# Kernel optimization log

Measured on AMD Instinct MI355X. Metric: run time of the kernel, lower is better.

The kernel has to match this reference:

```python
import jax, jax.numpy as jnp
import numpy as np

T = 8  # number of DP iterations (self.T)

def setup_inputs() -> dict:
    key = jax.random.key(0)
    ks = jax.random.split(key, 9)
    bs, dims, L, d = 16, 4, 2048, 256
    x = jax.random.uniform(ks[0], (bs, dims, L), dtype=jnp.float32)  # one-hot-like input
    s_in = 1.0 / np.sqrt(dims)
    s_d = 1.0 / np.sqrt(d)
    W1 = jax.random.uniform(ks[1], (d, dims), minval=-s_in, maxval=s_in, dtype=jnp.float32)
    b1 = jax.random.uniform(ks[2], (d,), minval=-s_in, maxval=s_in, dtype=jnp.float32)
    W2 = jax.random.uniform(ks[3], (d, d), minval=-s_d, maxval=s_d, dtype=jnp.float32)
    b2 = jax.random.uniform(ks[4], (d,), minval=-s_d, maxval=s_d, dtype=jnp.float32)
    W3 = jax.random.uniform(ks[5], (d, dims), minval=-s_in, maxval=s_in, dtype=jnp.float32)
    b3 = jax.random.uniform(ks[6], (d,), minval=-s_in, maxval=s_in, dtype=jnp.float32)
    W4 = jax.random.uniform(ks[7], (d, d), minval=-s_d, maxval=s_d, dtype=jnp.float32)
    b4 = jax.random.uniform(ks[8], (d,), minval=-s_d, maxval=s_d, dtype=jnp.float32)
    return dict(x=x, W1=W1, b1=b1, W2=W2, b2=b2, W3=W3, b3=b3, W4=W4, b4=b4)

def reference(x, W1, b1, W2, b2, W3, b3, W4, b4):
    # x: (bs, dims, L). The original allocates V:(bs,T+1,L+2,L+2,d) but only the
    # two diagonals V[i,j,j+1] ("up") and V[i,j,j-1] ("down") are ever written/read,
    # so the recurrence collapses to two (bs,L,d) lanes.
    a = jnp.einsum('bdl,od->blo', x, W1) + b1  # W1(x_j) for all j: (bs, L, d)
    bs, L, d = a.shape
    zcol = jnp.zeros((bs, 1, d), a.dtype)
    shift_r = lambda v: jnp.concatenate([zcol, v[:, :-1]], axis=1)  # v[j-1], zero at j=0
    shift_l = lambda v: jnp.concatenate([v[:, 1:], zcol], axis=1)   # v[j+1], zero at j=L-1
    up = jnp.zeros_like(a)   # up[j]   = V[i, j+1, j+2] (0-indexed lane)
    down = jnp.zeros_like(a) # down[j] = V[i, j+1, j]
    for _ in range(T):
        up = jax.nn.relu(a + shift_r(up) @ W2.T + b2)
        down = jax.nn.relu(a + shift_l(down) @ W2.T + b2)
    c = jnp.einsum('bdl,od->blo', x, W3) + b3
    # miu[j] = relu(W3 x_j + W4(V[T,j-1,j]) + W4(V[T,j+1,j]))
    miu = jax.nn.relu(c + (shift_r(up) @ W4.T + b4) + (shift_l(down) @ W4.T + b4))
    return miu  # (bs, L, d)
```

## Files before the change

kernel.cpp:

```cpp
#include <hip/hip_runtime.h>


typedef __bf16 bf16x8 __attribute__((ext_vector_type(8)));
typedef __bf16 bf16x4 __attribute__((ext_vector_type(4)));
typedef float f32x16 __attribute__((ext_vector_type(16)));

#define MFMA32(a, b, c) __builtin_amdgcn_mfma_f32_32x32x16_bf16(a, b, c, 0, 0, 0)

__device__ __forceinline__ unsigned short f2bf(float f) {
  unsigned int u = __builtin_bit_cast(unsigned int, f);
  u += 0x7fffu + ((u >> 16) & 1u);
  return (unsigned short)(u >> 16);
}

#define STATE_OFF 139264

__global__ void prep_kernel(const float* __restrict__ W1, const float* __restrict__ b1,
                            const float* __restrict__ W2, const float* __restrict__ b2,
                            const float* __restrict__ W3, const float* __restrict__ b3,
                            const float* __restrict__ W4, const float* __restrict__ b4,
                            unsigned short* __restrict__ ws) {
  int idx = blockIdx.x * 256 + threadIdx.x;
  if (idx >= 139264) return;
  float v = 0.0f;
  if (idx < 131072) {
    const float* W = (idx < 65536) ? W2 : W4;
    int i = idx & 65535;
    int j = i & 7, f = i >> 3;
    int lane = f & 63, slot = f >> 6;
    int ks = slot & 15, ot = slot >> 4;
    int o = ot * 32 + (lane & 31);
    int k = ks * 16 + (lane >> 5) * 8 + j;
    v = W[o * 256 + k];
  } else {
    int i = idx - 131072;
    bool first = (i < 4096);
    int ii = i & 4095;
    int j = ii & 7, f = ii >> 3;
    int lane = f & 63, ot = f >> 6;
    int o = ot * 32 + (lane & 31);
    if (lane < 32) {
      if (j < 4) v = first ? W1[o * 4 + j] : W3[o * 4 + j];
      else if (j == 4) v = first ? (b1[o] + b2[o]) : (b3[o] + 2.0f * b4[o]);
    }
  }
  ws[idx] = f2bf(v);
}

__global__ __launch_bounds__(256, 2)
void chain_kernel(const float* __restrict__ x, unsigned short* __restrict__ ws) {
  __shared__ int4 U[64 * 32];
  __shared__ int4 xw[80];
  __shared__ int4 zc;

  const int tid = threadIdx.x;
  const int l = tid & 63;
  const int w = tid >> 6;
  const int lane31 = l & 31;
  const int khalf = l >> 5;
  const int phase = blockIdx.x >> 9;
  const int tile = blockIdx.x & 511;
  const int b = tile >> 5;
  const int j0 = (tile & 31) * 64;

  const int4* w2f = (const int4*)ws;
  const int4* w1xg = (const int4*)(ws + 131072);

  if (tid == 0) zc = make_int4(0, 0, 0, 0);
  if (tid < 80) {
    int j = j0 - 8 + tid;
    int4 c = make_int4(0, 0, 0, 0);
    if (j >= 0 && j < 2048) {
      const float* xb = x + (b * 4) * 2048 + j;
      unsigned short h0 = f2bf(xb[0]);
      unsigned short h1 = f2bf(xb[2048]);
      unsigned short h2 = f2bf(xb[4096]);
      unsigned short h3 = f2bf(xb[6144]);
      c = make_int4((int)(h0 | ((unsigned int)h1 << 16)),
                    (int)(h2 | ((unsigned int)h3 << 16)),
                    0x00003f80, 0);
    }
    xw[tid] = c;
  }

  const int ot0 = w * 2;
  bf16x8 w2c[2][8];
  bf16x8 w1x[2];
#pragma unroll
  for (int t2 = 0; t2 < 2; ++t2) {
    w1x[t2] = __builtin_bit_cast(bf16x8, w1xg[(ot0 + t2) * 64 + l]);
#pragma unroll
    for (int ks = 0; ks < 8; ++ks)
      w2c[t2][ks] = __builtin_bit_cast(bf16x8, w2f[((ot0 + t2) * 16 + ks) * 64 + l]);
  }
  __syncthreads();

  const int mrow0 = lane31;
  const int mrow1 = 32 + lane31;

#pragma unroll 1
  for (int t = 1; t <= 8; ++t) {
    f32x16 acc[2][2] = {};
#pragma unroll
    for (int mt = 0; mt < 2; ++mt) {
      int m = mt ? mrow1 : mrow0;
      int widx = (phase == 0) ? (m + t - 1) : (m + 17 - t);
      const int4* p = (l < 32) ? (xw + widx) : (&zc);
      bf16x8 bx = __builtin_bit_cast(bf16x8, *p);
      acc[mt][0] = MFMA32(w1x[0], bx, acc[mt][0]);
      acc[mt][1] = MFMA32(w1x[1], bx, acc[mt][1]);
    }
    if (t > 1) {
#pragma unroll
      for (int ks = 0; ks < 16; ++ks) {
        int c0 = 2 * ks + khalf;
        bf16x8 bu0 = __builtin_bit_cast(bf16x8, U[mrow0 * 32 + (c0 ^ (mrow0 & 7))]);
        bf16x8 bu1 = __builtin_bit_cast(bf16x8, U[mrow1 * 32 + (c0 ^ (mrow1 & 7))]);
        bf16x8 af0, af1;
        if (ks < 8) { af0 = w2c[0][ks]; af1 = w2c[1][ks]; }
        else {
          af0 = __builtin_bit_cast(bf16x8, w2f[(ot0 * 16 + ks) * 64 + l]);
          af1 = __builtin_bit_cast(bf16x8, w2f[((ot0 + 1) * 16 + ks) * 64 + l]);
        }
        acc[0][0] = MFMA32(af0, bu0, acc[0][0]);
        acc[0][1] = MFMA32(af1, bu0, acc[0][1]);
        acc[1][0] = MFMA32(af0, bu1, acc[1][0]);
        acc[1][1] = MFMA32(af1, bu1, acc[1][1]);
      }
    }
    __syncthreads();
#pragma unroll
    for (int mt = 0; mt < 2; ++mt) {
      int row = mt ? mrow1 : mrow0;
#pragma unroll
      for (int t2 = 0; t2 < 2; ++t2) {
        int ot = ot0 + t2;
#pragma unroll
        for (int q = 0; q < 4; ++q) {
          bf16x4 h;
          h.x = (__bf16)fmaxf(acc[mt][t2][4 * q + 0], 0.0f);
          h.y = (__bf16)fmaxf(acc[mt][t2][4 * q + 1], 0.0f);
          h.z = (__bf16)fmaxf(acc[mt][t2][4 * q + 2], 0.0f);
          h.w = (__bf16)fmaxf(acc[mt][t2][4 * q + 3], 0.0f);
          int co = ot * 4 + q;
          int coff = row * 32 + (co ^ (row & 7));
          *(uint2*)((char*)(U + coff) + khalf * 8) = __builtin_bit_cast(uint2, h);
        }
      }
    }
    __syncthreads();
  }

  int4* stg = (int4*)(ws + STATE_OFF) + (phase * 512 + tile) * 2048;
#pragma unroll
  for (int i = 0; i < 8; ++i) stg[i * 256 + tid] = U[i * 256 + tid];
}

__global__ __launch_bounds__(256, 2)
void final_kernel(const float* __restrict__ x, const unsigned short* __restrict__ ws,
                  float* __restrict__ out) {
  __shared__ int4 S[2][64 * 32];
  __shared__ int4 xw[64];
  __shared__ int4 zc;

  const int tid = threadIdx.x;
  const int l = tid & 63;
  const int w = tid >> 6;
  const int lane31 = l & 31;
  const int khalf = l >> 5;
  const int tile = blockIdx.x;
  const int b = tile >> 5;
  const int j0 = (tile & 31) * 64;

  const int4* w4f = (const int4*)(ws + 65536);
  const int4* w3xg = (const int4*)(ws + 135168);
  const int4* stg = (const int4*)(ws + STATE_OFF);

  if (tid == 0) zc = make_int4(0, 0, 0, 0);
  if (tid < 64) {
    int j = j0 + tid;
    const float* xb = x + (b * 4) * 2048 + j;
    unsigned short h0 = f2bf(xb[0]);
    unsigned short h1 = f2bf(xb[2048]);
    unsigned short h2 = f2bf(xb[4096]);
    unsigned short h3 = f2bf(xb[6144]);
    xw[tid] = make_int4((int)(h0 | ((unsigned int)h1 << 16)),
                        (int)(h2 | ((unsigned int)h3 << 16)),
                        0x00003f80, 0);
  }
#pragma unroll
  for (int i = 0; i < 8; ++i) {
    S[0][i * 256 + tid] = stg[tile * 2048 + i * 256 + tid];
    S[1][i * 256 + tid] = stg[(512 + tile) * 2048 + i * 256 + tid];
  }
  __syncthreads();

  const int ot0 = w * 2;
  const int mrow0 = lane31;
  const int mrow1 = 32 + lane31;

  f32x16 acc[2][2] = {};
  bf16x8 w3x0 = __builtin_bit_cast(bf16x8, w3xg[ot0 * 64 + l]);
  bf16x8 w3x1 = __builtin_bit_cast(bf16x8, w3xg[(ot0 + 1) * 64 + l]);
#pragma unroll
  for (int mt = 0; mt < 2; ++mt) {
    int m = mt ? mrow1 : mrow0;
    const int4* p = (l < 32) ? (xw + m) : (&zc);
    bf16x8 bx = __builtin_bit_cast(bf16x8, *p);
    acc[mt][0] = MFMA32(w3x0, bx, acc[mt][0]);
    acc[mt][1] = MFMA32(w3x1, bx, acc[mt][1]);
  }
#pragma unroll 1
  for (int ph = 0; ph < 2; ++ph) {
    const int4* Sp = S[ph];
#pragma unroll
    for (int ks = 0; ks < 16; ++ks) {
      int c0 = 2 * ks + khalf;
      bf16x8 bu0 = __builtin_bit_cast(bf16x8, Sp[mrow0 * 32 + (c0 ^ (mrow0 & 7))]);
      bf16x8 bu1 = __builtin_bit_cast(bf16x8, Sp[mrow1 * 32 + (c0 ^ (mrow1 & 7))]);
      bf16x8 af0 = __builtin_bit_cast(bf16x8, w4f[(ot0 * 16 + ks) * 64 + l]);
      bf16x8 af1 = __builtin_bit_cast(bf16x8, w4f[((ot0 + 1) * 16 + ks) * 64 + l]);
      acc[0][0] = MFMA32(af0, bu0, acc[0][0]);
      acc[0][1] = MFMA32(af1, bu0, acc[0][1]);
      acc[1][0] = MFMA32(af0, bu1, acc[1][0]);
      acc[1][1] = MFMA32(af1, bu1, acc[1][1]);
    }
  }
#pragma unroll
  for (int mt = 0; mt < 2; ++mt) {
    int m = mt ? mrow1 : mrow0;
    int pbase = (b * 2048 + j0 + m) * 256;
#pragma unroll
    for (int t2 = 0; t2 < 2; ++t2) {
#pragma unroll
      for (int q = 0; q < 4; ++q) {
        int ob = (ot0 + t2) * 32 + 8 * q + 4 * khalf;
        float4 v;
        v.x = fmaxf(acc[mt][t2][4 * q + 0], 0.0f);
        v.y = fmaxf(acc[mt][t2][4 * q + 1], 0.0f);
        v.z = fmaxf(acc[mt][t2][4 * q + 2], 0.0f);
        v.w = fmaxf(acc[mt][t2][4 * q + 3], 0.0f);
        *(float4*)(out + pbase + ob) = v;
      }
    }
  }
}

extern "C" void kernel_launch(void* const* d_in, const int* in_sizes, int n_in,
                              void* d_out, int out_size, void* d_ws, size_t ws_size,
                              hipStream_t stream) {
  const float* x  = (const float*)d_in[0];
  const float* W1 = (const float*)d_in[1];
  const float* b1 = (const float*)d_in[2];
  const float* W2 = (const float*)d_in[3];
  const float* b2 = (const float*)d_in[4];
  const float* W3 = (const float*)d_in[5];
  const float* b3 = (const float*)d_in[6];
  const float* W4 = (const float*)d_in[7];
  const float* b4 = (const float*)d_in[8];
  unsigned short* ws = (unsigned short*)d_ws;

  prep_kernel<<<544, 256, 0, stream>>>(W1, b1, W2, b2, W3, b3, W4, b4, ws);
  chain_kernel<<<1024, 256, 0, stream>>>(x, ws);
  final_kernel<<<512, 256, 0, stream>>>(x, ws, (float*)d_out);
}
```

Measured before the change: 154.4 us.

## Re-partition chain kernel waves to keep full W2 slice in registers

Changes the per-wave work split in the chain kernel. Before, each wave covered 2 output tiles across both 32-row halves and reloaded half of its W2 fragments from global memory every iteration. Now each wave covers 4 output tiles for a single 32-row half, so its whole W2 slice (64 bf16x8 fragments) stays in registers and the per-step global reloads go away. In exchange, register pressure rises a lot under launch_bounds(256,2) and could spill. Each wave also reads half as many U rows from LDS.

```diff
diff --git a/kernel.cpp b/kernel.cpp
--- a/kernel.cpp
+++ b/kernel.cpp
@@ -58,6 +58,8 @@
   const int w = tid >> 6;
   const int lane31 = l & 31;
   const int khalf = l >> 5;
+  const int otg = w >> 1;
+  const int mhalf = w & 1;
   const int phase = blockIdx.x >> 9;
   const int tile = blockIdx.x & 511;
   const int b = tile >> 5;
@@ -83,69 +85,55 @@
     xw[tid] = c;
   }
 
-  const int ot0 = w * 2;
-  bf16x8 w2c[2][8];
-  bf16x8 w1x[2];
-#pragma unroll
-  for (int t2 = 0; t2 < 2; ++t2) {
-    w1x[t2] = __builtin_bit_cast(bf16x8, w1xg[(ot0 + t2) * 64 + l]);
-#pragma unroll
-    for (int ks = 0; ks < 8; ++ks)
-      w2c[t2][ks] = __builtin_bit_cast(bf16x8, w2f[((ot0 + t2) * 16 + ks) * 64 + l]);
+  bf16x8 w2c[4][16];
+  bf16x8 w1x[4];
+#pragma unroll
+  for (int i = 0; i < 4; ++i) {
+    int ot = otg * 4 + i;
+    w1x[i] = __builtin_bit_cast(bf16x8, w1xg[ot * 64 + l]);
+#pragma unroll
+    for (int ks = 0; ks < 16; ++ks)
+      w2c[i][ks] = __builtin_bit_cast(bf16x8, w2f[(ot * 16 + ks) * 64 + l]);
   }
   __syncthreads();
 
-  const int mrow0 = lane31;
-  const int mrow1 = 32 + lane31;
+  const int mrow = mhalf * 32 + lane31;
 
 #pragma unroll 1
   for (int t = 1; t <= 8; ++t) {
-    f32x16 acc[2][2] = {};
-#pragma unroll
-    for (int mt = 0; mt < 2; ++mt) {
-      int m = mt ? mrow1 : mrow0;
-      int widx = (phase == 0) ? (m + t - 1) : (m + 17 - t);
+    f32x16 acc[4] = {};
+    {
+      int widx = (phase == 0) ? (mrow + t - 1) : (mrow + 17 - t);
       const int4* p = (l < 32) ? (xw + widx) : (&zc);
       bf16x8 bx = __builtin_bit_cast(bf16x8, *p);
-      acc[mt][0] = MFMA32(w1x[0], bx, acc[mt][0]);
-      acc[mt][1] = MFMA32(w1x[1], bx, acc[mt][1]);
+#pragma unroll
+      for (int i = 0; i < 4; ++i) acc[i] = MFMA32(w1x[i], bx, acc[i]);
     }
     if (t > 1) {
 #pragma unroll
       for (int ks = 0; ks < 16; ++ks) {
         int c0 = 2 * ks + khalf;
-        bf16x8 bu0 = __builtin_bit_cast(bf16x8, U[mrow0 * 32 + (c0 ^ (mrow0 & 7))]);
-        bf16x8 bu1 = __builtin_bit_cast(bf16x8, U[mrow1 * 32 + (c0 ^ (mrow1 & 7))]);
-        bf16x8 af0, af1;
-        if (ks < 8) { af0 = w2c[0][ks]; af1 = w2c[1][ks]; }
-        else {
-          af0 = __builtin_bit_cast(bf16x8, w2f[(ot0 * 16 + ks) * 64 + l]);
-          af1 = __builtin_bit_cast(bf16x8, w2f[((ot0 + 1) * 16 + ks) * 64 + l]);
-        }
-        acc[0][0] = MFMA32(af0, bu0, acc[0][0]);
-        acc[0][1] = MFMA32(af1, bu0, acc[0][1]);
-        acc[1][0] = MFMA32(af0, bu1, acc[1][0]);
-        acc[1][1] = MFMA32(af1, bu1, acc[1][1]);
+        bf16x8 bu = __builtin_bit_cast(bf16x8, U[mrow * 32 + (c0 ^ (mrow & 7))]);
+        acc[0] = MFMA32(w2c[0][ks], bu, acc[0]);
+        acc[1] = MFMA32(w2c[1][ks], bu, acc[1]);
+        acc[2] = MFMA32(w2c[2][ks], bu, acc[2]);
+        acc[3] = MFMA32(w2c[3][ks], bu, acc[3]);
       }
     }
     __syncthreads();
 #pragma unroll
-    for (int mt = 0; mt < 2; ++mt) {
-      int row = mt ? mrow1 : mrow0;
-#pragma unroll
-      for (int t2 = 0; t2 < 2; ++t2) {
-        int ot = ot0 + t2;
-#pragma unroll
-        for (int q = 0; q < 4; ++q) {
-          bf16x4 h;
-          h.x = (__bf16)fmaxf(acc[mt][t2][4 * q + 0], 0.0f);
-          h.y = (__bf16)fmaxf(acc[mt][t2][4 * q + 1], 0.0f);
-          h.z = (__bf16)fmaxf(acc[mt][t2][4 * q + 2], 0.0f);
-          h.w = (__bf16)fmaxf(acc[mt][t2][4 * q + 3], 0.0f);
-          int co = ot * 4 + q;
-          int coff = row * 32 + (co ^ (row & 7));
-          *(uint2*)((char*)(U + coff) + khalf * 8) = __builtin_bit_cast(uint2, h);
-        }
+    for (int i = 0; i < 4; ++i) {
+      int ot = otg * 4 + i;
+#pragma unroll
+      for (int q = 0; q < 4; ++q) {
+        bf16x4 h;
+        h.x = (__bf16)fmaxf(acc[i][4 * q + 0], 0.0f);
+        h.y = (__bf16)fmaxf(acc[i][4 * q + 1], 0.0f);
+        h.z = (__bf16)fmaxf(acc[i][4 * q + 2], 0.0f);
+        h.w = (__bf16)fmaxf(acc[i][4 * q + 3], 0.0f);
+        int co = ot * 4 + q;
+        int coff = mrow * 32 + (co ^ (mrow & 7));
+        *(uint2*)((char*)(U + coff) + khalf * 8) = __builtin_bit_cast(uint2, h);
       }
     }
     __syncthreads();
```

Result: slower. 271.7 us (+75.9%).
